# Kernel optimization log

Measured on AMD Instinct MI355X. Metric: run time of the kernel, lower is better.

## Reference

```python
import jax, jax.numpy as jnp
import numpy as np

PATCH_SIZE = 128
IMG = 256


def _circle_perimeter(r_o, c_o, radius):
    # skimage.draw.circle_perimeter, method='bresenham' (midpoint circle),
    # including the duplicate octant-boundary points that skimage emits.
    rr, cc = [], []
    c, r = 0, radius
    d = 3 - 2 * radius
    while c <= r:
        rr += [r, -r, r, -r, c, -c, c, -c]
        cc += [c, c, -c, -c, r, r, -r, -r]
        if d < 0:
            d += 4 * c + 6
        else:
            d += 4 * (c - r) + 10
            r -= 1
        c += 1
    return np.asarray(rr) + r_o, np.asarray(cc) + c_o


def _radial_indices(patch_size, img):
    cy, cx = img // 2, img // 2
    rr_all, cc_all, seg_all = [], [], []
    for radius in range(1, patch_size - 1):  # radii 1..patch_size-2
        rr, cc = _circle_perimeter(cy, cx, radius)
        rr_all.append(rr)
        cc_all.append(cc)
        seg_all.append(np.full(rr.shape[0], radius - 1))
    return (np.concatenate(rr_all).astype(np.int32),
            np.concatenate(cc_all).astype(np.int32),
            np.concatenate(seg_all).astype(np.int32))


def setup_inputs() -> dict:
    key = jax.random.key(0)
    k1, k2 = jax.random.split(key)
    inp = jax.random.normal(k1, (64, 3, IMG, IMG), dtype=jnp.float32)
    tgt = jax.random.normal(k2, (64, 3, IMG, IMG), dtype=jnp.float32)
    w = np.float32(np.arange(0, 1, 1 / (PATCH_SIZE - 1)))  # length 127
    weights = jnp.asarray(w / np.sum(w))
    rr_idx, cc_idx, seg_ids = _radial_indices(PATCH_SIZE, IMG)
    return {"input": inp, "target": tgt, "weights": weights,
            "rr_idx": jnp.asarray(rr_idx), "cc_idx": jnp.asarray(cc_idx),
            "seg_ids": jnp.asarray(seg_ids)}


def reference(input, target, weights, rr_idx, cc_idx, seg_ids):
    B, C = input.shape[0], input.shape[1]
    R = weights.shape[0]          # patch_size - 1 curve bins
    nseg = R - 1                  # radii 1..patch_size-2
    f1 = jnp.fft.fft2(input)      # complex64 [B,C,H,W]
    f2 = jnp.fft.fft2(target)
    p1 = f1[:, :, rr_idx, cc_idx]  # [B,C,Ntot]
    p2 = f2[:, :, rr_idx, cc_idx]
    # original sums num/den over ALL dims (batch+channel+perimeter points)
    cross = jnp.sum(p1 * jnp.conj(p2), axis=(0, 1))        # [Ntot] complex
    pw1 = jnp.sum(jnp.abs(p1) ** 2, axis=(0, 1))           # [Ntot]
    pw2 = jnp.sum(jnp.abs(p2) ** 2, axis=(0, 1))
    num = jnp.abs(jax.ops.segment_sum(cross, seg_ids, num_segments=nseg))
    den = (jax.ops.segment_sum(pw1, seg_ids, num_segments=nseg) *
           jax.ops.segment_sum(pw2, seg_ids, num_segments=nseg))
    curve = jnp.concatenate([jnp.ones((1,), jnp.float32),
                             (num / jnp.sqrt(den)).astype(jnp.float32)])  # [R]
    # curve is identical across (b, c); Linear(R,1,bias=False) then total sum
    curve_full = jnp.broadcast_to(curve, (B, C, R))
    return jnp.sum(curve_full @ weights)
```

## Files before the change

kernel.cpp:

```cpp
#include <hip/hip_runtime.h>
#include <hip/hip_fp16.h>
#include <math.h>

#define NSEG 126
#define PI_F 3.14159265358979323846f

__device__ __forceinline__ unsigned bitrev8(unsigned v) { return __brev(v) >> 24; }
__device__ __forceinline__ unsigned bitrev6(unsigned v) { return __brev(v) >> 26; }
__device__ __forceinline__ float2 cmulc(float2 a, float2 b) {
    return make_float2(a.x*b.x - a.y*b.y, a.x*b.y + a.y*b.x);
}
__device__ __forceinline__ float2 mulmi(float2 a){ return make_float2(a.y, -a.x); }
__device__ __forceinline__ float2 h2f2(unsigned u) {
    __half2 h = __builtin_bit_cast(__half2, u);
    return __half22float2(h);
}
__device__ __forceinline__ unsigned f2h2(float2 v) {
    return __builtin_bit_cast(unsigned, __float22half2_rn(v));
}

#define BFLY(v, W) { float px_=__shfl_xor(v.x,HL), py_=__shfl_xor(v.y,HL); \
  if (up) { float dx_=px_-v.x, dy_=py_-v.y; v=make_float2(dx_*W.x-dy_*W.y, dx_*W.y+dy_*W.x); } \
  else    { v=make_float2(v.x+px_, v.y+py_); } }

#define ROW4(a,b,c,d) BFLY(a,w0) BFLY(b,w1) BFLY(c,w2) BFLY(d,w3)

#define FFT_STAGES(ALL) \
  { const int HL=32; const bool up=(lane&32)!=0; float s_,c_; \
    __sincosf(-PI_F*(float)(lane&31)*(1.0f/32.0f),&s_,&c_); \
    float2 w0=make_float2(c_,s_); \
    float2 w1=cmulc(w0,make_float2(0.99969882f,-0.02454123f)); \
    float2 w2=cmulc(w0,make_float2(0.99879546f,-0.04906767f)); \
    float2 w3=cmulc(w0,make_float2(0.99729046f,-0.07356456f)); ALL } \
  { const int HL=16; const bool up=(lane&16)!=0; float s_,c_; \
    __sincosf(-PI_F*(float)(lane&15)*(1.0f/16.0f),&s_,&c_); \
    float2 w0=make_float2(c_,s_); \
    float2 w1=cmulc(w0,make_float2(0.99879546f,-0.04906767f)); \
    float2 w2=cmulc(w0,make_float2(0.99518473f,-0.09801714f)); \
    float2 w3=cmulc(w0,make_float2(0.98917651f,-0.14673047f)); ALL } \
  { const int HL=8; const bool up=(lane&8)!=0; float s_,c_; \
    __sincosf(-PI_F*(float)(lane&7)*(1.0f/8.0f),&s_,&c_); \
    float2 w0=make_float2(c_,s_); \
    float2 w1=cmulc(w0,make_float2(0.99518473f,-0.09801714f)); \
    float2 w2=cmulc(w0,make_float2(0.98078528f,-0.19509032f)); \
    float2 w3=cmulc(w0,make_float2(0.95694034f,-0.29028468f)); ALL } \
  { const int HL=4; const bool up=(lane&4)!=0; float s_,c_; \
    __sincosf(-PI_F*(float)(lane&3)*(1.0f/4.0f),&s_,&c_); \
    float2 w0=make_float2(c_,s_); \
    float2 w1=cmulc(w0,make_float2(0.98078528f,-0.19509032f)); \
    float2 w2=cmulc(w0,make_float2(0.92387953f,-0.38268343f)); \
    float2 w3=cmulc(w0,make_float2(0.83146961f,-0.55557023f)); ALL } \
  { const int HL=2; const bool up=(lane&2)!=0; \
    float2 w0=(lane&1)?make_float2(0.f,-1.f):make_float2(1.f,0.f); \
    float2 w1=cmulc(w0,make_float2(0.92387953f,-0.38268343f)); \
    float2 w2=cmulc(w0,make_float2(0.70710678f,-0.70710678f)); \
    float2 w3=cmulc(w0,make_float2(0.38268343f,-0.92387953f)); ALL } \
  { const int HL=1; const bool up=(lane&1)!=0; \
    float2 w0=make_float2(1.f,0.f); \
    float2 w1=make_float2(0.70710678f,-0.70710678f); \
    float2 w2=make_float2(0.f,-1.f); \
    float2 w3=make_float2(-0.70710678f,-0.70710678f); ALL }

#define FIN(a0,a1,a2,a3) { float2 u_,v_; \
  u_=a0; v_=a2; a0=make_float2(u_.x+v_.x,u_.y+v_.y); a2=make_float2(u_.x-v_.x,u_.y-v_.y); \
  u_=a1; v_=a3; a1=make_float2(u_.x+v_.x,u_.y+v_.y); a3=mulmi(make_float2(u_.x-v_.x,u_.y-v_.y)); \
  u_=a0; v_=a1; a0=make_float2(u_.x+v_.x,u_.y+v_.y); a1=make_float2(u_.x-v_.x,u_.y-v_.y); \
  u_=a2; v_=a3; a2=make_float2(u_.x+v_.x,u_.y+v_.y); a3=make_float2(u_.x-v_.x,u_.y-v_.y); }

__global__ __launch_bounds__(1024) void prep_all(
    const int* __restrict__ rr, const int* __restrict__ cc,
    const int* __restrict__ seg, int n,
    int* __restrict__ starts, int* __restrict__ b_pack, float* __restrict__ acc)
{
    __shared__ int cnt[128];
    __shared__ int cur[128];
    int tid = threadIdx.x;
    if (tid < NSEG * 3) acc[tid] = 0.f;
    if (tid < 128) cnt[tid] = 0;
    __syncthreads();
    for (int i = tid; i < n; i += 1024) {
        int c = cc[i], r = rr[i];
        if ((c > 128) || (c == 128 && r > 128)) atomicAdd(&cnt[255 - c], 1);
    }
    __syncthreads();
    if (tid < 64) {
        int2 c2 = reinterpret_cast<const int2*>(cnt)[tid];
        int lsum = c2.x + c2.y;
        int pre = lsum;
        #pragma unroll
        for (int off = 1; off < 64; off <<= 1) {
            int v = __shfl_up(pre, off);
            if (tid >= off) pre += v;
        }
        int excl = pre - lsum;
        int2 outv = make_int2(excl, excl + c2.x);
        reinterpret_cast<int2*>(cur)[tid] = outv;
        reinterpret_cast<int2*>(starts)[tid] = outv;
        if (tid == 63) starts[128] = excl + c2.x + c2.y;
    }
    __syncthreads();
    for (int i = tid; i < n; i += 1024) {
        int c = cc[i], r = rr[i];
        if ((c > 128) || (c == 128 && r > 128)) {
            int j = 255 - c;
            int pos = atomicAdd(&cur[j], 1);
            b_pack[pos] = r | (((256 - r) & 255) << 8) | (seg[i] << 16);
        }
    }
}

#define ALL4 ROW4(x00,x01,x02,x03) ROW4(x10,x11,x12,x13) \
             ROW4(x20,x21,x22,x23) ROW4(x30,x31,x32,x33)

__global__ __launch_bounds__(512, 1) void rowfft_kernel(
    const float* __restrict__ inp, const float* __restrict__ tgt,
    unsigned* __restrict__ G, int pair_base)
{
    __shared__ unsigned T[256 * 17];
    int tid    = threadIdx.x;
    int wv     = tid >> 6;
    int lane   = tid & 63;
    int plocal = blockIdx.x >> 3;
    int rowgrp = blockIdx.x & 7;
    int row0   = (rowgrp << 5) + (wv << 2);
    size_t base = (((size_t)(pair_base + plocal)) << 16) + ((size_t)row0 << 8);
    const float4* s1 = (const float4*)(inp + base);
    const float4* s2 = (const float4*)(tgt + base);

    float4 A0 = s1[lane],       B0 = s2[lane];
    float4 A1 = s1[64 + lane],  B1 = s2[64 + lane];
    float4 A2 = s1[128 + lane], B2 = s2[128 + lane];
    float4 A3 = s1[192 + lane], B3 = s2[192 + lane];
    float2 x00 = make_float2(A0.x, B0.x), x01 = make_float2(A0.y, B0.y),
           x02 = make_float2(A0.z, B0.z), x03 = make_float2(A0.w, B0.w);
    float2 x10 = make_float2(A1.x, B1.x), x11 = make_float2(A1.y, B1.y),
           x12 = make_float2(A1.z, B1.z), x13 = make_float2(A1.w, B1.w);
    float2 x20 = make_float2(A2.x, B2.x), x21 = make_float2(A2.y, B2.y),
           x22 = make_float2(A2.z, B2.z), x23 = make_float2(A2.w, B2.w);
    float2 x30 = make_float2(A3.x, B3.x), x31 = make_float2(A3.y, B3.y),
           x32 = make_float2(A3.z, B3.z), x33 = make_float2(A3.w, B3.w);

    FFT_STAGES(ALL4)
    FIN(x00,x01,x02,x03) FIN(x10,x11,x12,x13)
    FIN(x20,x21,x22,x23) FIN(x30,x31,x32,x33)

    unsigned* dst = G + (((size_t)plocal) << 16) + (rowgrp << 5);
    #pragma unroll
    for (int pass = 0; pass < 2; pass++) {
        if ((wv >> 2) == pass) {
            int xr = ((wv & 3) << 2);
            unsigned* Tp = &T[(4 * lane) * 17 + xr];
            Tp[0]  = f2h2(x00); Tp[17] = f2h2(x01); Tp[34] = f2h2(x02); Tp[51] = f2h2(x03);
            Tp[1]  = f2h2(x10); Tp[18] = f2h2(x11); Tp[35] = f2h2(x12); Tp[52] = f2h2(x13);
            Tp[2]  = f2h2(x20); Tp[19] = f2h2(x21); Tp[36] = f2h2(x22); Tp[53] = f2h2(x23);
            Tp[3]  = f2h2(x30); Tp[20] = f2h2(x31); Tp[37] = f2h2(x32); Tp[54] = f2h2(x33);
        }
        __syncthreads();
        int xl = tid & 15;
        int qq = tid >> 4;
        #pragma unroll
        for (int ii = 0; ii < 8; ii++) {
            int q = qq + (ii << 5);
            dst[q * 256 + (pass << 4) + xl] = T[q * 17 + xl];
        }
        __syncthreads();
    }
}

#define ALL8 ROW4(x00,x01,x02,x03) ROW4(x10,x11,x12,x13) \
             ROW4(x20,x21,x22,x23) ROW4(x30,x31,x32,x33) \
             ROW4(x40,x41,x42,x43) ROW4(x50,x51,x52,x53) \
             ROW4(x60,x61,x62,x63) ROW4(x70,x71,x72,x73)

#define STORE_GATHER(t, A0,A1,A2,A3, B0,B1,B2,B3) { \
    slot[nb]       = A0; slot[nb + 128]       = A1; \
    slot[nb + 64]  = A2; slot[nb + 192]       = A3; \
    slot[256 + nb] = B0; slot[256 + nb + 128] = B1; \
    slot[256 + nb + 64] = B2; slot[256 + nb + 192] = B3; \
    int j_ = jb0 + (t); \
    int s0_ = starts[j_], s1_ = starts[j_ + 1]; \
    int e_  = s0_ + lane; \
    int pk_ = (e_ < s1_) ? b_pack[e_] : 0; \
    while (e_ < s1_) { \
        int e2_  = e_ + 64; \
        int pk2_ = (e2_ < s1_) ? b_pack[e2_] : 0; \
        float2 a_ = slot[256 + (pk_ & 255)]; \
        float2 m_ = slot[(pk_ >> 8) & 255]; \
        int sg_ = pk_ >> 16; \
        float f1x_ = a_.x + m_.x, f1y_ = a_.y - m_.y; \
        float dx_  = a_.x - m_.x, dy_  = a_.y + m_.y; \
        atomicAdd(&accl[sg_ * 3 + 0], f1x_ * dy_ - f1y_ * dx_); \
        atomicAdd(&accl[sg_ * 3 + 1], f1x_ * f1x_ + f1y_ * f1y_); \
        atomicAdd(&accl[sg_ * 3 + 2], dx_ * dx_ + dy_ * dy_); \
        e_ = e2_; pk_ = pk2_; \
    } }

__global__ __launch_bounds__(512, 1) void colfft_gather_kernel(
    const unsigned* __restrict__ G, const int* __restrict__ starts,
    const int* __restrict__ b_pack, float* __restrict__ acc)
{
    __shared__ float2 Fb[8 * 512];
    __shared__ float accl[NSEG * 3];
    int tid    = threadIdx.x;
    int wv     = tid >> 6;
    int lane   = tid & 63;
    int plocal = blockIdx.x >> 2;
    int b      = blockIdx.x & 3;
    int jb0    = (b << 5) + (wv << 2);

    for (int i = tid; i < NSEG * 3; i += 512) accl[i] = 0.f;
    __syncthreads();

    const unsigned* Gp = G + (((size_t)plocal) << 16);
    const uint4* cA = (const uint4*)(Gp + ((size_t)bitrev8((unsigned)(jb0 + 1)) << 8));
    const uint4* cB = (const uint4*)(Gp + ((size_t)bitrev8((unsigned)(255 - jb0)) << 8));
    const uint4* cC = (const uint4*)(Gp + ((size_t)bitrev8((unsigned)(jb0 + 2)) << 8));
    const uint4* cD = (const uint4*)(Gp + ((size_t)bitrev8((unsigned)(254 - jb0)) << 8));
    const uint4* cE = (const uint4*)(Gp + ((size_t)bitrev8((unsigned)(jb0 + 3)) << 8));
    const uint4* cF = (const uint4*)(Gp + ((size_t)bitrev8((unsigned)(253 - jb0)) << 8));
    const uint4* cG = (const uint4*)(Gp + ((size_t)bitrev8((unsigned)(jb0 + 4)) << 8));
    const uint4* cH = (const uint4*)(Gp + ((size_t)bitrev8((unsigned)(252 - jb0)) << 8));
    uint4 rA = cA[lane], rB = cB[lane], rC = cC[lane], rD = cD[lane];
    uint4 rE = cE[lane], rF = cF[lane], rG = cG[lane], rH = cH[lane];

    float2 x00 = h2f2(rA.x), x01 = h2f2(rA.y), x02 = h2f2(rA.z), x03 = h2f2(rA.w);
    float2 x10 = h2f2(rB.x), x11 = h2f2(rB.y), x12 = h2f2(rB.z), x13 = h2f2(rB.w);
    float2 x20 = h2f2(rC.x), x21 = h2f2(rC.y), x22 = h2f2(rC.z), x23 = h2f2(rC.w);
    float2 x30 = h2f2(rD.x), x31 = h2f2(rD.y), x32 = h2f2(rD.z), x33 = h2f2(rD.w);
    float2 x40 = h2f2(rE.x), x41 = h2f2(rE.y), x42 = h2f2(rE.z), x43 = h2f2(rE.w);
    float2 x50 = h2f2(rF.x), x51 = h2f2(rF.y), x52 = h2f2(rF.z), x53 = h2f2(rF.w);
    float2 x60 = h2f2(rG.x), x61 = h2f2(rG.y), x62 = h2f2(rG.z), x63 = h2f2(rG.w);
    float2 x70 = h2f2(rH.x), x71 = h2f2(rH.y), x72 = h2f2(rH.z), x73 = h2f2(rH.w);

    FFT_STAGES(ALL8)
    FIN(x00,x01,x02,x03) FIN(x10,x11,x12,x13)
    FIN(x20,x21,x22,x23) FIN(x30,x31,x32,x33)
    FIN(x40,x41,x42,x43) FIN(x50,x51,x52,x53)
    FIN(x60,x61,x62,x63) FIN(x70,x71,x72,x73)

    float2* slot = Fb + (wv << 9);
    int nb = (int)bitrev6((unsigned)lane);
    STORE_GATHER(0, x00,x01,x02,x03, x10,x11,x12,x13)
    STORE_GATHER(1, x20,x21,x22,x23, x30,x31,x32,x33)
    STORE_GATHER(2, x40,x41,x42,x43, x50,x51,x52,x53)
    STORE_GATHER(3, x60,x61,x62,x63, x70,x71,x72,x73)
    __syncthreads();

    for (int i = tid; i < NSEG * 3; i += 512) {
        float v = accl[i];
        if (v != 0.f) atomicAdd(&acc[i], v);
    }
}

__global__ void final_kernel(const float* __restrict__ acc, const float* __restrict__ w,
                             float* __restrict__ out, float scale) {
    int lane = threadIdx.x;
    float val = 0.f;
    for (int s = lane; s < NSEG; s += 64) {
        float cr = acc[s * 3 + 0];
        float p1 = acc[s * 3 + 1];
        float p2 = acc[s * 3 + 2];
        float den = p1 * p2;
        float curve = den > 0.f ? fabsf(cr) * rsqrtf(den) : 0.f;
        val += curve * w[s + 1];
    }
    if (lane == 0) val += w[0];
    #pragma unroll
    for (int off = 32; off > 0; off >>= 1) val += __shfl_down(val, off);
    if (lane == 0) out[0] = scale * val;
}

extern "C" void kernel_launch(void* const* d_in, const int* in_sizes, int n_in,
                              void* d_out, int out_size, void* d_ws, size_t ws_size,
                              hipStream_t stream)
{
    const float* inp = (const float*)d_in[0];
    const float* tgt = (const float*)d_in[1];
    const float* wts = (const float*)d_in[2];
    const int*   rr  = (const int*)d_in[3];
    const int*   cc  = (const int*)d_in[4];
    const int*   sg  = (const int*)d_in[5];
    int npts   = in_sizes[3];
    int npairs = in_sizes[0] >> 16;

    char* ws = (char*)d_ws;
    float* acc    = (float*)(ws + 0);
    int*   starts = (int*)(ws + 2048);
    int*   b_pack = (int*)(ws + 4096);
    size_t goff = 4096 + (size_t)npts * 4;
    goff = (goff + 255) & ~(size_t)255;
    unsigned* G = (unsigned*)(ws + goff);

    size_t per_pair = (size_t)256 * 256 * 4;
    int maxchunk = (int)((ws_size > goff ? (ws_size - goff) : 0) / per_pair);
    if (maxchunk < 1) maxchunk = 1;
    if (maxchunk > npairs) maxchunk = npairs;

    prep_all<<<1, 1024, 0, stream>>>(rr, cc, sg, npts, starts, b_pack, acc);

    for (int pb = 0; pb < npairs; pb += maxchunk) {
        int cp = npairs - pb < maxchunk ? npairs - pb : maxchunk;
        rowfft_kernel<<<cp * 8, 512, 0, stream>>>(inp, tgt, G, pb);
        colfft_gather_kernel<<<cp * 4, 512, 0, stream>>>(G, starts, b_pack, acc);
    }

    final_kernel<<<1, 64, 0, stream>>>(acc, wts, (float*)d_out, (float)npairs);
}
```

Measured before the change: 240.0 us.

## Replace column FFT with fp16 MFMA DFT matmul against precomputed twiddle matrix

The shuffle-based radix-2 column FFT is replaced by a dense 256-point DFT done as complex matrix multiplies on MFMA 16x16x32 fp16 instructions. The twiddle matrix is built once per call by a new prep kernel and kept in workspace. Each block now handles a whole pair, looping over 8 column groups and gathering perimeter points from shared memory. This trades the O(N log N) FFT for O(N^2) matrix work on the matrix cores, and cuts the grid to one block per pair, which may leave the GPU underoccupied. It also adds fp16 rounding to the twiddles.

```diff
diff --git a/kernel.cpp b/kernel.cpp
--- a/kernel.cpp
+++ b/kernel.cpp
@@ -5,18 +5,21 @@
 #define NSEG 126
 #define PI_F 3.14159265358979323846f
 
+typedef _Float16 f16x8 __attribute__((ext_vector_type(8)));
+typedef float f32x4 __attribute__((ext_vector_type(4)));
+#define MFMA(A,B,C) __builtin_amdgcn_mfma_f32_16x16x32_f16(A,B,C,0,0,0)
+
 __device__ __forceinline__ unsigned bitrev8(unsigned v) { return __brev(v) >> 24; }
-__device__ __forceinline__ unsigned bitrev6(unsigned v) { return __brev(v) >> 26; }
 __device__ __forceinline__ float2 cmulc(float2 a, float2 b) {
     return make_float2(a.x*b.x - a.y*b.y, a.x*b.y + a.y*b.x);
 }
 __device__ __forceinline__ float2 mulmi(float2 a){ return make_float2(a.y, -a.x); }
-__device__ __forceinline__ float2 h2f2(unsigned u) {
-    __half2 h = __builtin_bit_cast(__half2, u);
-    return __half22float2(h);
-}
 __device__ __forceinline__ unsigned f2h2(float2 v) {
     return __builtin_bit_cast(unsigned, __float22half2_rn(v));
+}
+__device__ __forceinline__ f16x8 pack4u(unsigned a, unsigned b, unsigned c, unsigned d) {
+    uint4 u = make_uint4(a, b, c, d);
+    return __builtin_bit_cast(f16x8, u);
 }
 
 #define BFLY(v, W) { float px_=__shfl_xor(v.x,HL), py_=__shfl_xor(v.y,HL); \
@@ -109,6 +112,31 @@
     }
 }
 
+__global__ __launch_bounds__(512) void prep_w(uint4* __restrict__ AWr,
+                                              uint4* __restrict__ AWi)
+{
+    int gid  = blockIdx.x * 512 + threadIdx.x;
+    int l    = gid & 63;
+    int tile = gid >> 6;
+    int mt = tile >> 3, ks = tile & 7;
+    int u  = mt * 16 + (l & 15);
+    int kb = ks * 32 + ((l >> 4) << 3);
+    unsigned wr[8], wi[8];
+    #pragma unroll
+    for (int j = 0; j < 8; j++) {
+        int t8 = (u * (kb + j)) & 255;
+        float ang = (float)t8 * (2.0f * PI_F / 256.0f);
+        float cs, sn;
+        __sincosf(ang, &sn, &cs);
+        wr[j] = (unsigned)__builtin_bit_cast(unsigned short, (_Float16)cs);
+        wi[j] = (unsigned)__builtin_bit_cast(unsigned short, (_Float16)(-sn));
+    }
+    AWr[gid] = make_uint4(wr[0]|(wr[1]<<16), wr[2]|(wr[3]<<16),
+                          wr[4]|(wr[5]<<16), wr[6]|(wr[7]<<16));
+    AWi[gid] = make_uint4(wi[0]|(wi[1]<<16), wi[2]|(wi[3]<<16),
+                          wi[4]|(wi[5]<<16), wi[6]|(wi[7]<<16));
+}
+
 #define ALL4 ROW4(x00,x01,x02,x03) ROW4(x10,x11,x12,x13) \
              ROW4(x20,x21,x22,x23) ROW4(x30,x31,x32,x33)
 
@@ -131,6 +159,7 @@
     float4 A1 = s1[64 + lane],  B1 = s2[64 + lane];
     float4 A2 = s1[128 + lane], B2 = s2[128 + lane];
     float4 A3 = s1[192 + lane], B3 = s2[192 + lane];
+
     float2 x00 = make_float2(A0.x, B0.x), x01 = make_float2(A0.y, B0.y),
            x02 = make_float2(A0.z, B0.z), x03 = make_float2(A0.w, B0.w);
     float2 x10 = make_float2(A1.x, B1.x), x11 = make_float2(A1.y, B1.y),
@@ -167,83 +196,132 @@
     }
 }
 
-#define ALL8 ROW4(x00,x01,x02,x03) ROW4(x10,x11,x12,x13) \
-             ROW4(x20,x21,x22,x23) ROW4(x30,x31,x32,x33) \
-             ROW4(x40,x41,x42,x43) ROW4(x50,x51,x52,x53) \
-             ROW4(x60,x61,x62,x63) ROW4(x70,x71,x72,x73)
-
-#define STORE_GATHER(t, A0,A1,A2,A3, B0,B1,B2,B3) { \
-    slot[nb]       = A0; slot[nb + 128]       = A1; \
-    slot[nb + 64]  = A2; slot[nb + 192]       = A3; \
-    slot[256 + nb] = B0; slot[256 + nb + 128] = B1; \
-    slot[256 + nb + 64] = B2; slot[256 + nb + 192] = B3; \
-    int j_ = jb0 + (t); \
-    int s0_ = starts[j_], s1_ = starts[j_ + 1]; \
-    int e_  = s0_ + lane; \
-    int pk_ = (e_ < s1_) ? b_pack[e_] : 0; \
-    while (e_ < s1_) { \
-        int e2_  = e_ + 64; \
-        int pk2_ = (e2_ < s1_) ? b_pack[e2_] : 0; \
-        float2 a_ = slot[256 + (pk_ & 255)]; \
-        float2 m_ = slot[(pk_ >> 8) & 255]; \
-        int sg_ = pk_ >> 16; \
-        float f1x_ = a_.x + m_.x, f1y_ = a_.y - m_.y; \
-        float dx_  = a_.x - m_.x, dy_  = a_.y + m_.y; \
-        atomicAdd(&accl[sg_ * 3 + 0], f1x_ * dy_ - f1y_ * dx_); \
-        atomicAdd(&accl[sg_ * 3 + 1], f1x_ * f1x_ + f1y_ * f1y_); \
-        atomicAdd(&accl[sg_ * 3 + 2], dx_ * dx_ + dy_ * dy_); \
-        e_ = e2_; pk_ = pk2_; \
-    } }
-
-__global__ __launch_bounds__(512, 1) void colfft_gather_kernel(
-    const unsigned* __restrict__ G, const int* __restrict__ starts,
+__global__ __launch_bounds__(512, 1) void colfft_mfma_kernel(
+    const unsigned* __restrict__ G, const uint4* __restrict__ AWr,
+    const uint4* __restrict__ AWi, const int* __restrict__ starts,
     const int* __restrict__ b_pack, float* __restrict__ acc)
 {
-    __shared__ float2 Fb[8 * 512];
+    __shared__ float2 sL[16 * 257];
+    __shared__ float2 sH[16 * 257];
     __shared__ float accl[NSEG * 3];
-    int tid    = threadIdx.x;
-    int wv     = tid >> 6;
-    int lane   = tid & 63;
-    int plocal = blockIdx.x >> 2;
-    int b      = blockIdx.x & 3;
-    int jb0    = (b << 5) + (wv << 2);
+    int tid  = threadIdx.x;
+    int wv   = tid >> 6;
+    int lane = tid & 63;
+    int l15  = lane & 15;
+    int g8   = (lane >> 4) << 3;
+    const unsigned* Gp = G + (((size_t)blockIdx.x) << 16);
 
     for (int i = tid; i < NSEG * 3; i += 512) accl[i] = 0.f;
-    __syncthreads();
-
-    const unsigned* Gp = G + (((size_t)plocal) << 16);
-    const uint4* cA = (const uint4*)(Gp + ((size_t)bitrev8((unsigned)(jb0 + 1)) << 8));
-    const uint4* cB = (const uint4*)(Gp + ((size_t)bitrev8((unsigned)(255 - jb0)) << 8));
-    const uint4* cC = (const uint4*)(Gp + ((size_t)bitrev8((unsigned)(jb0 + 2)) << 8));
-    const uint4* cD = (const uint4*)(Gp + ((size_t)bitrev8((unsigned)(254 - jb0)) << 8));
-    const uint4* cE = (const uint4*)(Gp + ((size_t)bitrev8((unsigned)(jb0 + 3)) << 8));
-    const uint4* cF = (const uint4*)(Gp + ((size_t)bitrev8((unsigned)(253 - jb0)) << 8));
-    const uint4* cG = (const uint4*)(Gp + ((size_t)bitrev8((unsigned)(jb0 + 4)) << 8));
-    const uint4* cH = (const uint4*)(Gp + ((size_t)bitrev8((unsigned)(252 - jb0)) << 8));
-    uint4 rA = cA[lane], rB = cB[lane], rC = cC[lane], rD = cD[lane];
-    uint4 rE = cE[lane], rF = cF[lane], rG = cG[lane], rH = cH[lane];
-
-    float2 x00 = h2f2(rA.x), x01 = h2f2(rA.y), x02 = h2f2(rA.z), x03 = h2f2(rA.w);
-    float2 x10 = h2f2(rB.x), x11 = h2f2(rB.y), x12 = h2f2(rB.z), x13 = h2f2(rB.w);
-    float2 x20 = h2f2(rC.x), x21 = h2f2(rC.y), x22 = h2f2(rC.z), x23 = h2f2(rC.w);
-    float2 x30 = h2f2(rD.x), x31 = h2f2(rD.y), x32 = h2f2(rD.z), x33 = h2f2(rD.w);
-    float2 x40 = h2f2(rE.x), x41 = h2f2(rE.y), x42 = h2f2(rE.z), x43 = h2f2(rE.w);
-    float2 x50 = h2f2(rF.x), x51 = h2f2(rF.y), x52 = h2f2(rF.z), x53 = h2f2(rF.w);
-    float2 x60 = h2f2(rG.x), x61 = h2f2(rG.y), x62 = h2f2(rG.z), x63 = h2f2(rG.w);
-    float2 x70 = h2f2(rH.x), x71 = h2f2(rH.y), x72 = h2f2(rH.z), x73 = h2f2(rH.w);
-
-    FFT_STAGES(ALL8)
-    FIN(x00,x01,x02,x03) FIN(x10,x11,x12,x13)
-    FIN(x20,x21,x22,x23) FIN(x30,x31,x32,x33)
-    FIN(x40,x41,x42,x43) FIN(x50,x51,x52,x53)
-    FIN(x60,x61,x62,x63) FIN(x70,x71,x72,x73)
-
-    float2* slot = Fb + (wv << 9);
-    int nb = (int)bitrev6((unsigned)lane);
-    STORE_GATHER(0, x00,x01,x02,x03, x10,x11,x12,x13)
-    STORE_GATHER(1, x20,x21,x22,x23, x30,x31,x32,x33)
-    STORE_GATHER(2, x40,x41,x42,x43, x50,x51,x52,x53)
-    STORE_GATHER(3, x60,x61,x62,x63, x70,x71,x72,x73)
+
+    int mt0 = wv << 1, mt1 = mt0 + 1;
+
+    for (int p = 0; p < 8; p++) {
+        __syncthreads();
+        int cbL = 16 * p + 1;
+        int cbH = 240 - 16 * p;
+        const unsigned* rowL = Gp + (size_t)bitrev8((unsigned)(cbL + l15)) * 256;
+        const unsigned* rowH = Gp + (size_t)bitrev8((unsigned)(cbH + l15)) * 256;
+
+        f32x4 aR0L = {0,0,0,0}, aI0L = {0,0,0,0}, aR0H = {0,0,0,0}, aI0H = {0,0,0,0};
+        f32x4 aR1L = {0,0,0,0}, aI1L = {0,0,0,0}, aR1H = {0,0,0,0}, aI1H = {0,0,0,0};
+
+        #pragma unroll
+        for (int ks = 0; ks < 8; ks++) {
+            int koff = ks * 32 + g8;
+            uint4 bL0 = *(const uint4*)(rowL + koff);
+            uint4 bL1 = *(const uint4*)(rowL + koff + 4);
+            uint4 bH0 = *(const uint4*)(rowH + koff);
+            uint4 bH1 = *(const uint4*)(rowH + koff + 4);
+            uint4 wr0 = AWr[((mt0 << 3) + ks) * 64 + lane];
+            uint4 wi0 = AWi[((mt0 << 3) + ks) * 64 + lane];
+            uint4 wr1 = AWr[((mt1 << 3) + ks) * 64 + lane];
+            uint4 wi1 = AWi[((mt1 << 3) + ks) * 64 + lane];
+
+            f16x8 GrL = pack4u((bL0.x & 0xffffu) | (bL0.y << 16),
+                               (bL0.z & 0xffffu) | (bL0.w << 16),
+                               (bL1.x & 0xffffu) | (bL1.y << 16),
+                               (bL1.z & 0xffffu) | (bL1.w << 16));
+            unsigned giL0 = (bL0.x >> 16) | (bL0.y & 0xffff0000u);
+            unsigned giL1 = (bL0.z >> 16) | (bL0.w & 0xffff0000u);
+            unsigned giL2 = (bL1.x >> 16) | (bL1.y & 0xffff0000u);
+            unsigned giL3 = (bL1.z >> 16) | (bL1.w & 0xffff0000u);
+            f16x8 GiL  = pack4u(giL0, giL1, giL2, giL3);
+            f16x8 nGiL = pack4u(giL0 ^ 0x80008000u, giL1 ^ 0x80008000u,
+                                giL2 ^ 0x80008000u, giL3 ^ 0x80008000u);
+            f16x8 GrH = pack4u((bH0.x & 0xffffu) | (bH0.y << 16),
+                               (bH0.z & 0xffffu) | (bH0.w << 16),
+                               (bH1.x & 0xffffu) | (bH1.y << 16),
+                               (bH1.z & 0xffffu) | (bH1.w << 16));
+            unsigned giH0 = (bH0.x >> 16) | (bH0.y & 0xffff0000u);
+            unsigned giH1 = (bH0.z >> 16) | (bH0.w & 0xffff0000u);
+            unsigned giH2 = (bH1.x >> 16) | (bH1.y & 0xffff0000u);
+            unsigned giH3 = (bH1.z >> 16) | (bH1.w & 0xffff0000u);
+            f16x8 GiH  = pack4u(giH0, giH1, giH2, giH3);
+            f16x8 nGiH = pack4u(giH0 ^ 0x80008000u, giH1 ^ 0x80008000u,
+                                giH2 ^ 0x80008000u, giH3 ^ 0x80008000u);
+
+            f16x8 Wr0 = __builtin_bit_cast(f16x8, wr0);
+            f16x8 Wi0 = __builtin_bit_cast(f16x8, wi0);
+            f16x8 Wr1 = __builtin_bit_cast(f16x8, wr1);
+            f16x8 Wi1 = __builtin_bit_cast(f16x8, wi1);
+
+            aR0L = MFMA(Wr0, GrL, aR0L);  aR0L = MFMA(Wi0, nGiL, aR0L);
+            aI0L = MFMA(Wr0, GiL, aI0L);  aI0L = MFMA(Wi0, GrL,  aI0L);
+            aR0H = MFMA(Wr0, GrH, aR0H);  aR0H = MFMA(Wi0, nGiH, aR0H);
+            aI0H = MFMA(Wr0, GiH, aI0H);  aI0H = MFMA(Wi0, GrH,  aI0H);
+            aR1L = MFMA(Wr1, GrL, aR1L);  aR1L = MFMA(Wi1, nGiL, aR1L);
+            aI1L = MFMA(Wr1, GiL, aI1L);  aI1L = MFMA(Wi1, GrL,  aI1L);
+            aR1H = MFMA(Wr1, GrH, aR1H);  aR1H = MFMA(Wi1, nGiH, aR1H);
+            aI1H = MFMA(Wr1, GiH, aI1H);  aI1H = MFMA(Wi1, GrH,  aI1H);
+        }
+
+        {
+            int cw  = l15 * 257;
+            int rb0 = mt0 * 16 + ((lane >> 4) << 2);
+            int rb1 = mt1 * 16 + ((lane >> 4) << 2);
+            sL[cw + rb0 + 0] = make_float2(aR0L.x, aI0L.x);
+            sL[cw + rb0 + 1] = make_float2(aR0L.y, aI0L.y);
+            sL[cw + rb0 + 2] = make_float2(aR0L.z, aI0L.z);
+            sL[cw + rb0 + 3] = make_float2(aR0L.w, aI0L.w);
+            sH[cw + rb0 + 0] = make_float2(aR0H.x, aI0H.x);
+            sH[cw + rb0 + 1] = make_float2(aR0H.y, aI0H.y);
+            sH[cw + rb0 + 2] = make_float2(aR0H.z, aI0H.z);
+            sH[cw + rb0 + 3] = make_float2(aR0H.w, aI0H.w);
+            sL[cw + rb1 + 0] = make_float2(aR1L.x, aI1L.x);
+            sL[cw + rb1 + 1] = make_float2(aR1L.y, aI1L.y);
+            sL[cw + rb1 + 2] = make_float2(aR1L.z, aI1L.z);
+            sL[cw + rb1 + 3] = make_float2(aR1L.w, aI1L.w);
+            sH[cw + rb1 + 0] = make_float2(aR1H.x, aI1H.x);
+            sH[cw + rb1 + 1] = make_float2(aR1H.y, aI1H.y);
+            sH[cw + rb1 + 2] = make_float2(aR1H.z, aI1H.z);
+            sH[cw + rb1 + 3] = make_float2(aR1H.w, aI1H.w);
+        }
+        __syncthreads();
+
+        #pragma unroll
+        for (int t = 0; t < 2; t++) {
+            int jj = (wv << 1) + t;
+            int j_ = (p << 4) + jj;
+            const float2* Fhi = sH + (15 - jj) * 257;
+            const float2* Flo = sL + jj * 257;
+            int s0 = starts[j_], s1 = starts[j_ + 1];
+            int e  = s0 + lane;
+            int pk = (e < s1) ? b_pack[e] : 0;
+            while (e < s1) {
+                int e2  = e + 64;
+                int pk2 = (e2 < s1) ? b_pack[e2] : 0;
+                float2 a = Fhi[pk & 255];
+                float2 m = Flo[(pk >> 8) & 255];
+                int sg = pk >> 16;
+                float f1x = a.x + m.x, f1y = a.y - m.y;
+                float dx  = a.x - m.x, dy  = a.y + m.y;
+                atomicAdd(&accl[sg * 3 + 0], f1x * dy - f1y * dx);
+                atomicAdd(&accl[sg * 3 + 1], f1x * f1x + f1y * f1y);
+                atomicAdd(&accl[sg * 3 + 2], dx * dx + dy * dy);
+                e = e2; pk = pk2;
+            }
+        }
+    }
     __syncthreads();
 
     for (int i = tid; i < NSEG * 3; i += 512) {
@@ -287,8 +365,11 @@
     float* acc    = (float*)(ws + 0);
     int*   starts = (int*)(ws + 2048);
     int*   b_pack = (int*)(ws + 4096);
-    size_t goff = 4096 + (size_t)npts * 4;
-    goff = (goff + 255) & ~(size_t)255;
+    size_t awoff = 4096 + (size_t)npts * 4;
+    awoff = (awoff + 255) & ~(size_t)255;
+    uint4* AWr = (uint4*)(ws + awoff);
+    uint4* AWi = (uint4*)(ws + awoff + 131072);
+    size_t goff = awoff + 262144;
     unsigned* G = (unsigned*)(ws + goff);
 
     size_t per_pair = (size_t)256 * 256 * 4;
@@ -297,11 +378,12 @@
     if (maxchunk > npairs) maxchunk = npairs;
 
     prep_all<<<1, 1024, 0, stream>>>(rr, cc, sg, npts, starts, b_pack, acc);
+    prep_w<<<16, 512, 0, stream>>>(AWr, AWi);
 
     for (int pb = 0; pb < npairs; pb += maxchunk) {
         int cp = npairs - pb < maxchunk ? npairs - pb : maxchunk;
         rowfft_kernel<<<cp * 8, 512, 0, stream>>>(inp, tgt, G, pb);
-        colfft_gather_kernel<<<cp * 4, 512, 0, stream>>>(G, starts, b_pack, acc);
+        colfft_mfma_kernel<<<cp, 512, 0, stream>>>(G, AWr, AWi, starts, b_pack, acc);
     }
 
     final_kernel<<<1, 64, 0, stream>>>(acc, wts, (float*)d_out, (float)npairs);
```

Result: slower. 277.5 us (+15.6%).
